# Performance work log

Measured on AMD Instinct MI355X. Metric: run time of the kernel, lower is better.

The kernel has to match this reference:

```python
import jax, jax.numpy as jnp
import numpy as np

N = 10000          # nodes
E = 160000         # edges (before self-loops)
F_IN = 256
H, C = 8, 64       # heads, channels per head
NUM_CLASSES = 40
NEG_SLOPE = 0.2    # PyG GATConv default leaky_relu slope


def setup_inputs() -> dict:
    key = jax.random.key(0)
    ks = jax.random.split(key, 16)
    s = 0.1  # keep logits tame
    x = jax.random.normal(ks[0], (N, F_IN), jnp.float32)
    edge_index = jax.random.randint(ks[1], (2, E), 0, N)
    W0 = jax.random.normal(ks[2], (F_IN, H * C), jnp.float32) / np.sqrt(F_IN)
    a_src0 = jax.random.normal(ks[3], (H, C), jnp.float32) * s
    a_dst0 = jax.random.normal(ks[4], (H, C), jnp.float32) * s
    b0 = jnp.zeros((H * C,), jnp.float32)
    W1 = jax.random.normal(ks[5], (H * C, H * C), jnp.float32) / np.sqrt(H * C)
    a_src1 = jax.random.normal(ks[6], (H, C), jnp.float32) * s
    a_dst1 = jax.random.normal(ks[7], (H, C), jnp.float32) * s
    b1 = jnp.zeros((H * C,), jnp.float32)
    W2 = jax.random.normal(ks[8], (H * C, NUM_CLASSES), jnp.float32) / np.sqrt(H * C)
    a_src2 = jax.random.normal(ks[9], (1, NUM_CLASSES), jnp.float32) * s
    a_dst2 = jax.random.normal(ks[10], (1, NUM_CLASSES), jnp.float32) * s
    b2 = jnp.zeros((NUM_CLASSES,), jnp.float32)
    return dict(x=x, edge_index=edge_index, W0=W0, a_src0=a_src0, a_dst0=a_dst0, b0=b0,
                W1=W1, a_src1=a_src1, a_dst1=a_dst1, b1=b1,
                W2=W2, a_src2=a_src2, a_dst2=a_dst2, b2=b2)


def gat_conv(x, src, dst, W, a_src, a_dst, b, concat):
    """PyG GATConv (eval mode: dropout = identity)."""
    n = x.shape[0]
    h, c = a_src.shape
    hx = (x @ W).reshape(n, h, c)                       # [N,H,C]
    al_s = jnp.sum(hx * a_src, axis=-1)                 # [N,H]
    al_d = jnp.sum(hx * a_dst, axis=-1)                 # [N,H]
    e = jax.nn.leaky_relu(al_s[src] + al_d[dst], NEG_SLOPE)  # [E,H]
    # neighbor softmax over incoming edges of each dst node
    m = jax.ops.segment_max(e, dst, num_segments=n)     # [N,H]
    ex = jnp.exp(e - m[dst])
    denom = jax.ops.segment_sum(ex, dst, num_segments=n)
    alpha = ex / (denom[dst] + 1e-16)                   # [E,H]
    msg = hx[src] * alpha[:, :, None]                   # [E,H,C]
    out = jax.ops.segment_sum(msg, dst, num_segments=n) # [N,H,C]
    out = out.reshape(n, h * c) if concat else out.mean(axis=1)
    return out + b


def reference(x, edge_index, W0, a_src0, a_dst0, b0, W1, a_src1, a_dst1, b1,
              W2, a_src2, a_dst2, b2):
    # add self-loops once (PyG GATConv add_self_loops=True)
    loops = jnp.arange(N, dtype=edge_index.dtype)
    src = jnp.concatenate([edge_index[0], loops])
    dst = jnp.concatenate([edge_index[1], loops])
    x = jax.nn.elu(gat_conv(x, src, dst, W0, a_src0, a_dst0, b0, True))
    x = jax.nn.elu(gat_conv(x, src, dst, W1, a_src1, a_dst1, b1, True))
    return gat_conv(x, src, dst, W2, a_src2, a_dst2, b2, False)
```

## Files before the change

### kernel.cpp

```cpp
#include <hip/hip_runtime.h>
#include <math.h>

#define NN 10000
#define EE 160000
#define ET 170000
#define FIN 256
#define HH 8
#define CC 64
#define HC 512
#define NCLS 40
#define ELLW 96

typedef unsigned short u16;
typedef unsigned int u32;
typedef _Float16 f16;
using f16x8 = __attribute__((ext_vector_type(8))) _Float16;
using f16x4 = __attribute__((ext_vector_type(4))) _Float16;
using f32x4 = __attribute__((ext_vector_type(4))) float;

#define MFMA16(a, b, c) __builtin_amdgcn_mfma_f32_16x16x32_f16((a), (b), (c), 0, 0, 0)

__global__ __launch_bounds__(256) void prep_kernel(const float* __restrict__ x,
                                                   const float* __restrict__ W0,
                                                   const float* __restrict__ W1,
                                                   const float* __restrict__ W2,
                                                   f16* __restrict__ xh,
                                                   f16* __restrict__ w0T,
                                                   f16* __restrict__ w1T,
                                                   f16* __restrict__ w2T,
                                                   int* __restrict__ cnt) {
    int i = blockIdx.x * 256 + threadIdx.x;
    if (i < NN) cnt[i] = 0;
    if (i < NN * FIN / 4) {
        float4 v = ((const float4*)x)[i];
        f16x4 o;
        o[0] = (f16)v.x; o[1] = (f16)v.y; o[2] = (f16)v.z; o[3] = (f16)v.w;
        ((f16x4*)xh)[i] = o;
    } else {
        int j = i - NN * FIN / 4;
        if (j < HC * FIN) {
            int n = j >> 8, k = j & 255;
            w0T[j] = (f16)W0[(size_t)k * HC + n];
        } else if (j < HC * FIN + HC * HC) {
            int q = j - HC * FIN;
            int n = q >> 9, k = q & 511;
            w1T[q] = (f16)W1[(size_t)k * HC + n];
        } else if (j < HC * FIN + HC * HC + NCLS * HC) {
            int q = j - HC * FIN - HC * HC;
            int n = q >> 9, k = q & 511;
            w2T[q] = (f16)W2[(size_t)k * NCLS + n];
        }
    }
}

__global__ __launch_bounds__(256) void scatter_ell(const int* __restrict__ ei,
                                                   int* __restrict__ cnt,
                                                   int* __restrict__ ell) {
    int e = blockIdx.x * 256 + threadIdx.x;
    if (e >= ET) return;
    int s, d;
    if (e < EE) { s = ei[e]; d = ei[EE + e]; }
    else        { s = e - EE; d = s; }
    int pos = atomicAdd(&cnt[d], 1);
    if (pos < ELLW) ell[(size_t)d * ELLW + pos] = s;
}

template <int K>
__global__ __launch_bounds__(512) void gemm_attn(const f16* __restrict__ A,
                                                 const f16* __restrict__ BT,
                                                 const float* __restrict__ a_src,
                                                 const float* __restrict__ a_dst,
                                                 f16* __restrict__ hx2,
                                                 float* __restrict__ al_s,
                                                 float* __restrict__ al_d) {
    constexpr int KK = K / 32;
    constexpr int CH = K / 8;
    __shared__ f16 Bs[64 * K];
    int t = threadIdx.x;
    int hp = blockIdx.x;
    int lane = t & 63, w = t >> 6;
    int fm = lane & 15, g = lane >> 4;
    int bm = blockIdx.y * 128 + w * 16;
    int row = bm + fm;
    bool rok = row < NN;

    f16x8 af[KK];
#pragma unroll
    for (int kk = 0; kk < KK; ++kk) {
        uint4 r = rok ? *(const uint4*)(A + (size_t)row * K + kk * 32 + g * 8)
                      : make_uint4(0u, 0u, 0u, 0u);
        af[kk] = __builtin_bit_cast(f16x8, r);
    }

    for (int sl = 0; sl < 2; ++sl) {
        int h = hp * 2 + sl;
        const f16* bsrc = BT + (size_t)h * 64 * K;
        for (int c = t; c < 64 * CH; c += 512) {
            int brow = c / CH;
            int j = c - brow * CH;
            uint4 v = *(const uint4*)(bsrc + (size_t)brow * K + j * 8);
            *(uint4*)&Bs[(size_t)brow * K + ((j ^ (brow & 7)) * 8)] = v;
        }
        __syncthreads();

        f32x4 acc[4] = {};
#pragma unroll
        for (int kk = 0; kk < KK; ++kk) {
#pragma unroll
            for (int nt = 0; nt < 4; ++nt) {
                f16x8 b = *(const f16x8*)
                    &Bs[(nt * 16 + fm) * K + (((kk * 4 + g) ^ (fm & 7)) * 8)];
                acc[nt] = MFMA16(af[kk], b, acc[nt]);
            }
        }

        float asc[4], adc[4];
#pragma unroll
        for (int nt = 0; nt < 4; ++nt) {
            asc[nt] = a_src[h * 64 + nt * 16 + fm];
            adc[nt] = a_dst[h * 64 + nt * 16 + fm];
        }
#pragma unroll
        for (int r = 0; r < 4; ++r) {
            int orow = bm + g * 4 + r;
            float s = acc[0][r] * asc[0] + acc[1][r] * asc[1] +
                      acc[2][r] * asc[2] + acc[3][r] * asc[3];
            float d = acc[0][r] * adc[0] + acc[1][r] * adc[1] +
                      acc[2][r] * adc[2] + acc[3][r] * adc[3];
#pragma unroll
            for (int off = 1; off < 16; off <<= 1) {
                s += __shfl_xor(s, off);
                d += __shfl_xor(d, off);
            }
            if (orow < NN) {
                if (fm == 0) {
                    al_s[orow * 8 + h] = s;
                    al_d[orow * 8 + h] = d;
                }
#pragma unroll
                for (int nt = 0; nt < 4; ++nt)
                    hx2[(size_t)orow * HC + h * 64 + nt * 16 + fm] =
                        (f16)acc[nt][r];
            }
        }
        __syncthreads();
    }
}

__global__ __launch_bounds__(256) void gemm2_attn(const f16* __restrict__ A,
                                                  const f16* __restrict__ BT,
                                                  const float* __restrict__ a_src2,
                                                  const float* __restrict__ a_dst2,
                                                  float* __restrict__ hx40,
                                                  float* __restrict__ als2,
                                                  float* __restrict__ ald2) {
    __shared__ f16 Bs[48 * HC];
    int t = threadIdx.x;
    int lane = t & 63, w = t >> 6;
    int fm = lane & 15, g = lane >> 4;
    int bm = blockIdx.x * 64 + w * 16;
    int row = bm + fm;
    bool rok = row < NN;

    for (int c = t; c < 48 * 64; c += 256) {
        int brow = c >> 6, j = c & 63;
        uint4 v = make_uint4(0u, 0u, 0u, 0u);
        if (brow < NCLS) v = *(const uint4*)(BT + (size_t)brow * HC + j * 8);
        *(uint4*)&Bs[brow * HC + ((j ^ (brow & 7)) * 8)] = v;
    }

    f16x8 af[16];
#pragma unroll
    for (int kk = 0; kk < 16; ++kk) {
        uint4 r = rok ? *(const uint4*)(A + (size_t)row * HC + kk * 32 + g * 8)
                      : make_uint4(0u, 0u, 0u, 0u);
        af[kk] = __builtin_bit_cast(f16x8, r);
    }
    __syncthreads();

    f32x4 acc[3] = {};
#pragma unroll
    for (int kk = 0; kk < 16; ++kk) {
#pragma unroll
        for (int nt = 0; nt < 3; ++nt) {
            f16x8 b = *(const f16x8*)
                &Bs[(nt * 16 + fm) * HC + (((kk * 4 + g) ^ (fm & 7)) * 8)];
            acc[nt] = MFMA16(af[kk], b, acc[nt]);
        }
    }

    float a2s[3], a2d[3];
#pragma unroll
    for (int nt = 0; nt < 3; ++nt) {
        int col = nt * 16 + fm;
        a2s[nt] = (col < NCLS) ? a_src2[col] : 0.f;
        a2d[nt] = (col < NCLS) ? a_dst2[col] : 0.f;
    }
#pragma unroll
    for (int r = 0; r < 4; ++r) {
        int orow = bm + g * 4 + r;
        float s = acc[0][r] * a2s[0] + acc[1][r] * a2s[1] + acc[2][r] * a2s[2];
        float d = acc[0][r] * a2d[0] + acc[1][r] * a2d[1] + acc[2][r] * a2d[2];
#pragma unroll
        for (int off = 1; off < 16; off <<= 1) {
            s += __shfl_xor(s, off);
            d += __shfl_xor(d, off);
        }
        if (orow < NN) {
            if (fm == 0) { als2[orow] = s; ald2[orow] = d; }
#pragma unroll
            for (int nt = 0; nt < 3; ++nt) {
                int col = nt * 16 + fm;
                if (col < NCLS) hx40[(size_t)orow * NCLS + col] = acc[nt][r];
            }
        }
    }
}

__global__ __launch_bounds__(256) void agg_ell(const f16* __restrict__ hx2,
                                               const float* __restrict__ al_s,
                                               const float* __restrict__ al_d,
                                               const int* __restrict__ cnt,
                                               const int* __restrict__ ell,
                                               const float* __restrict__ bias,
                                               f16* __restrict__ outF) {
    __shared__ float accbuf[2][64][8];
    __shared__ float denbuf[2][64];
    int t = threadIdx.x;
    int lane = t & 63, w = t >> 6;
    int p = w >> 1, sub = w & 1;
    int n = blockIdx.x * 2 + p;
    bool nok = n < NN;
    int ch = lane * 8;
    int h = lane >> 3;
    float acc[8] = {0.f, 0.f, 0.f, 0.f, 0.f, 0.f, 0.f, 0.f};
    float den = 0.f;
    if (nok) {
        float ald = al_d[n * HH + h];
        int dg = cnt[n]; if (dg > ELLW) dg = ELLW;
        const int* ep = ell + (size_t)n * ELLW;
        int nq = dg >> 2;
        for (int q = sub; q < nq; q += 2) {
            int4 ss = *(const int4*)(ep + (q << 2));
            float e0 = al_s[ss.x * HH + h], e1 = al_s[ss.y * HH + h];
            float e2 = al_s[ss.z * HH + h], e3 = al_s[ss.w * HH + h];
            uint4 v0 = *(const uint4*)(hx2 + (size_t)ss.x * HC + ch);
            uint4 v1 = *(const uint4*)(hx2 + (size_t)ss.y * HC + ch);
            uint4 v2 = *(const uint4*)(hx2 + (size_t)ss.z * HC + ch);
            uint4 v3 = *(const uint4*)(hx2 + (size_t)ss.w * HC + ch);
            e0 += ald; e0 = e0 > 0.f ? e0 : 0.2f * e0;
            e1 += ald; e1 = e1 > 0.f ? e1 : 0.2f * e1;
            e2 += ald; e2 = e2 > 0.f ? e2 : 0.2f * e2;
            e3 += ald; e3 = e3 > 0.f ? e3 : 0.2f * e3;
            float w0 = __expf(e0), w1 = __expf(e1);
            float w2 = __expf(e2), w3 = __expf(e3);
            f16x8 f0 = __builtin_bit_cast(f16x8, v0);
            f16x8 f1 = __builtin_bit_cast(f16x8, v1);
            f16x8 f2 = __builtin_bit_cast(f16x8, v2);
            f16x8 f3 = __builtin_bit_cast(f16x8, v3);
#pragma unroll
            for (int j = 0; j < 8; ++j)
                acc[j] += w0 * (float)f0[j] + w1 * (float)f1[j] +
                          w2 * (float)f2[j] + w3 * (float)f3[j];
            den += w0 + w1 + w2 + w3;
        }
        if (sub == (nq & 1)) {
            for (int i = nq << 2; i < dg; ++i) {
                int s = ep[i];
                float e = al_s[s * HH + h] + ald;
                e = e > 0.f ? e : 0.2f * e;
                float wgt = __expf(e);
                uint4 v = *(const uint4*)(hx2 + (size_t)s * HC + ch);
                f16x8 f = __builtin_bit_cast(f16x8, v);
#pragma unroll
                for (int j = 0; j < 8; ++j) acc[j] += wgt * (float)f[j];
                den += wgt;
            }
        }
    }
    if (sub == 1) {
#pragma unroll
        for (int j = 0; j < 8; ++j) accbuf[p][lane][j] = acc[j];
        denbuf[p][lane] = den;
    }
    __syncthreads();
    if (sub == 0 && nok) {
#pragma unroll
        for (int j = 0; j < 8; ++j) acc[j] += accbuf[p][lane][j];
        den += denbuf[p][lane];
        float inv = 1.f / (den + 1e-16f);
        float4 b0v = *(const float4*)(bias + ch);
        float4 b1v = *(const float4*)(bias + ch + 4);
        float bb[8] = {b0v.x, b0v.y, b0v.z, b0v.w, b1v.x, b1v.y, b1v.z, b1v.w};
        f16x8 o;
#pragma unroll
        for (int j = 0; j < 8; ++j) {
            float v = acc[j] * inv + bb[j];
            v = v > 0.f ? v : expm1f(v);
            o[j] = (f16)v;
        }
        *(uint4*)(outF + (size_t)n * HC + ch) = __builtin_bit_cast(uint4, o);
    }
}

__global__ __launch_bounds__(64) void agg2_final(const float* __restrict__ hx40,
                                                 const float* __restrict__ als,
                                                 const float* __restrict__ aldp,
                                                 const int* __restrict__ cnt,
                                                 const int* __restrict__ ell,
                                                 const float* __restrict__ b2,
                                                 float* __restrict__ out) {
    int n = blockIdx.x;
    int c = threadIdx.x;
    float ald = aldp[n];
    int dg = cnt[n]; if (dg > ELLW) dg = ELLW;
    const int* ep = ell + (size_t)n * ELLW;
    float acc = 0.f, den = 0.f;
    int i = 0;
    for (; i + 4 <= dg; i += 4) {
        int4 ss = *(const int4*)(ep + i);
        float e0 = als[ss.x], e1 = als[ss.y], e2 = als[ss.z], e3 = als[ss.w];
        float v0 = 0.f, v1 = 0.f, v2 = 0.f, v3 = 0.f;
        if (c < NCLS) {
            v0 = hx40[(size_t)ss.x * NCLS + c];
            v1 = hx40[(size_t)ss.y * NCLS + c];
            v2 = hx40[(size_t)ss.z * NCLS + c];
            v3 = hx40[(size_t)ss.w * NCLS + c];
        }
        e0 += ald; e0 = e0 > 0.f ? e0 : 0.2f * e0;
        e1 += ald; e1 = e1 > 0.f ? e1 : 0.2f * e1;
        e2 += ald; e2 = e2 > 0.f ? e2 : 0.2f * e2;
        e3 += ald; e3 = e3 > 0.f ? e3 : 0.2f * e3;
        float w0 = __expf(e0), w1 = __expf(e1), w2 = __expf(e2), w3 = __expf(e3);
        acc += w0 * v0 + w1 * v1 + w2 * v2 + w3 * v3;
        den += w0 + w1 + w2 + w3;
    }
    for (; i < dg; ++i) {
        int s = ep[i];
        float e = als[s] + ald;
        e = e > 0.f ? e : 0.2f * e;
        float wgt = __expf(e);
        if (c < NCLS) acc += wgt * hx40[(size_t)s * NCLS + c];
        den += wgt;
    }
    if (c < NCLS) out[(size_t)n * NCLS + c] = acc / (den + 1e-16f) + b2[c];
}

extern "C" void kernel_launch(void* const* d_in, const int* in_sizes, int n_in,
                              void* d_out, int out_size, void* d_ws, size_t ws_size,
                              hipStream_t stream) {
    const float* x   = (const float*)d_in[0];
    const int*   ei  = (const int*)  d_in[1];
    const float* W0  = (const float*)d_in[2];
    const float* as0 = (const float*)d_in[3];
    const float* ad0 = (const float*)d_in[4];
    const float* b0  = (const float*)d_in[5];
    const float* W1  = (const float*)d_in[6];
    const float* as1 = (const float*)d_in[7];
    const float* ad1 = (const float*)d_in[8];
    const float* b1  = (const float*)d_in[9];
    const float* W2  = (const float*)d_in[10];
    const float* as2 = (const float*)d_in[11];
    const float* ad2 = (const float*)d_in[12];
    const float* b2  = (const float*)d_in[13];
    float* out = (float*)d_out;

    char* p = (char*)d_ws;
    int* cnt  = (int*)p; p += 40064;
    int* ell  = (int*)p; p += (size_t)NN * ELLW * 4;
    f16* w0T  = (f16*)p; p += HC * FIN * 2;
    f16* w1T  = (f16*)p; p += HC * HC * 2;
    f16* w2T  = (f16*)p; p += NCLS * HC * 2;
    f16* xh   = (f16*)p; p += (size_t)NN * FIN * 2;
    f16* hxA  = (f16*)p; p += (size_t)NN * HC * 2;
    f16* hxB  = (f16*)p; p += (size_t)NN * HC * 2;
    f16* fA   = (f16*)p; p += (size_t)NN * HC * 2;
    f16* fB   = (f16*)p; p += (size_t)NN * HC * 2;
    float* hx40 = (float*)p; p += (size_t)NN * NCLS * 4;
    float* als0 = (float*)p; p += NN * HH * 4;
    float* ald0 = (float*)p; p += NN * HH * 4;
    float* als1 = (float*)p; p += NN * HH * 4;
    float* ald1 = (float*)p; p += NN * HH * 4;
    float* als2 = (float*)p; p += NN * 4;
    float* ald2 = (float*)p; p += NN * 4;

    const int NBR = (NN + 127) / 128;
    const int NAG = (NN + 1) / 2;
    const int NB2 = (NN + 63) / 64;
    const int PREP = NN * FIN / 4 + HC * FIN + HC * HC + NCLS * HC;

    prep_kernel<<<(PREP + 255) / 256, 256, 0, stream>>>(
        x, W0, W1, W2, xh, w0T, w1T, w2T, cnt);
    scatter_ell<<<(ET + 255) / 256, 256, 0, stream>>>(ei, cnt, ell);

    dim3 gA(4, NBR);
    gemm_attn<FIN><<<gA, 512, 0, stream>>>(xh, w0T, as0, ad0, hxA, als0, ald0);
    agg_ell<<<NAG, 256, 0, stream>>>(hxA, als0, ald0, cnt, ell, b0, fA);
    gemm_attn<HC><<<gA, 512, 0, stream>>>(fA, w1T, as1, ad1, hxB, als1, ald1);
    agg_ell<<<NAG, 256, 0, stream>>>(hxB, als1, ald1, cnt, ell, b1, fB);
    gemm2_attn<<<NB2, 256, 0, stream>>>(fB, w2T, as2, ad2, hx40, als2, ald2);
    agg2_final<<<NN, 64, 0, stream>>>(hx40, als2, ald2, cnt, ell, b2, out);
}
```

Baseline: 206.5 us.

## Split layer aggregation into column slices with intra-wave edge parallelism

Replaces the two-wave-per-node aggregation with a kernel where each wave handles one node and one 128-column slice (two heads), and a 4-slice grid dimension covers all columns. Within a wave, four edge groups of 16 lanes process edges in parallel and are combined with cross-lane shuffles, removing the shared-memory reduction and __syncthreads. This aims to expose more independent gathers per wave and better spread work over CUs. In exchange, each edge's index and attention logit are reloaded per slice, and the grid assumes NN divisible by 4, dropping the bounds check.

```diff
diff --git a/kernel.cpp b/kernel.cpp
--- a/kernel.cpp
+++ b/kernel.cpp
@@ -6,13 +6,10 @@
 #define ET 170000
 #define FIN 256
 #define HH 8
-#define CC 64
 #define HC 512
 #define NCLS 40
 #define ELLW 96
 
-typedef unsigned short u16;
-typedef unsigned int u32;
 typedef _Float16 f16;
 using f16x8 = __attribute__((ext_vector_type(8))) _Float16;
 using f16x4 = __attribute__((ext_vector_type(4))) _Float16;
@@ -217,80 +214,63 @@
     }
 }
 
-__global__ __launch_bounds__(256) void agg_ell(const f16* __restrict__ hx2,
-                                               const float* __restrict__ al_s,
-                                               const float* __restrict__ al_d,
-                                               const int* __restrict__ cnt,
-                                               const int* __restrict__ ell,
-                                               const float* __restrict__ bias,
-                                               f16* __restrict__ outF) {
-    __shared__ float accbuf[2][64][8];
-    __shared__ float denbuf[2][64];
+__global__ __launch_bounds__(256) void agg_slice(const f16* __restrict__ hx2,
+                                                 const float* __restrict__ al_s,
+                                                 const float* __restrict__ al_d,
+                                                 const int* __restrict__ cnt,
+                                                 const int* __restrict__ ell,
+                                                 const float* __restrict__ bias,
+                                                 f16* __restrict__ outF) {
     int t = threadIdx.x;
     int lane = t & 63, w = t >> 6;
-    int p = w >> 1, sub = w & 1;
-    int n = blockIdx.x * 2 + p;
-    bool nok = n < NN;
-    int ch = lane * 8;
-    int h = lane >> 3;
+    int li = lane & 15, eg = lane >> 4;
+    int s = blockIdx.y;
+    int n = blockIdx.x * 4 + w;
+    int h = s * 2 + (li >> 3);
+    int co = s * 128 + li * 8;
+    float ald = al_d[n * HH + h];
+    int dg = cnt[n]; if (dg > ELLW) dg = ELLW;
+    const int* ep = ell + (size_t)n * ELLW;
     float acc[8] = {0.f, 0.f, 0.f, 0.f, 0.f, 0.f, 0.f, 0.f};
     float den = 0.f;
-    if (nok) {
-        float ald = al_d[n * HH + h];
-        int dg = cnt[n]; if (dg > ELLW) dg = ELLW;
-        const int* ep = ell + (size_t)n * ELLW;
-        int nq = dg >> 2;
-        for (int q = sub; q < nq; q += 2) {
-            int4 ss = *(const int4*)(ep + (q << 2));
-            float e0 = al_s[ss.x * HH + h], e1 = al_s[ss.y * HH + h];
-            float e2 = al_s[ss.z * HH + h], e3 = al_s[ss.w * HH + h];
-            uint4 v0 = *(const uint4*)(hx2 + (size_t)ss.x * HC + ch);
-            uint4 v1 = *(const uint4*)(hx2 + (size_t)ss.y * HC + ch);
-            uint4 v2 = *(const uint4*)(hx2 + (size_t)ss.z * HC + ch);
-            uint4 v3 = *(const uint4*)(hx2 + (size_t)ss.w * HC + ch);
-            e0 += ald; e0 = e0 > 0.f ? e0 : 0.2f * e0;
-            e1 += ald; e1 = e1 > 0.f ? e1 : 0.2f * e1;
-            e2 += ald; e2 = e2 > 0.f ? e2 : 0.2f * e2;
-            e3 += ald; e3 = e3 > 0.f ? e3 : 0.2f * e3;
-            float w0 = __expf(e0), w1 = __expf(e1);
-            float w2 = __expf(e2), w3 = __expf(e3);
-            f16x8 f0 = __builtin_bit_cast(f16x8, v0);
-            f16x8 f1 = __builtin_bit_cast(f16x8, v1);
-            f16x8 f2 = __builtin_bit_cast(f16x8, v2);
-            f16x8 f3 = __builtin_bit_cast(f16x8, v3);
-#pragma unroll
-            for (int j = 0; j < 8; ++j)
-                acc[j] += w0 * (float)f0[j] + w1 * (float)f1[j] +
-                          w2 * (float)f2[j] + w3 * (float)f3[j];
-            den += w0 + w1 + w2 + w3;
-        }
-        if (sub == (nq & 1)) {
-            for (int i = nq << 2; i < dg; ++i) {
-                int s = ep[i];
-                float e = al_s[s * HH + h] + ald;
-                e = e > 0.f ? e : 0.2f * e;
-                float wgt = __expf(e);
-                uint4 v = *(const uint4*)(hx2 + (size_t)s * HC + ch);
-                f16x8 f = __builtin_bit_cast(f16x8, v);
-#pragma unroll
-                for (int j = 0; j < 8; ++j) acc[j] += wgt * (float)f[j];
-                den += wgt;
-            }
-        }
-    }
-    if (sub == 1) {
-#pragma unroll
-        for (int j = 0; j < 8; ++j) accbuf[p][lane][j] = acc[j];
-        denbuf[p][lane] = den;
-    }
-    __syncthreads();
-    if (sub == 0 && nok) {
-#pragma unroll
-        for (int j = 0; j < 8; ++j) acc[j] += accbuf[p][lane][j];
-        den += denbuf[p][lane];
+    int i = eg;
+    for (; i + 4 < dg; i += 8) {
+        int s0 = ep[i], s1 = ep[i + 4];
+        float e0 = al_s[s0 * HH + h], e1 = al_s[s1 * HH + h];
+        uint4 v0 = *(const uint4*)(hx2 + (size_t)s0 * HC + co);
+        uint4 v1 = *(const uint4*)(hx2 + (size_t)s1 * HC + co);
+        e0 += ald; e0 = e0 > 0.f ? e0 : 0.2f * e0;
+        e1 += ald; e1 = e1 > 0.f ? e1 : 0.2f * e1;
+        float w0 = __expf(e0), w1 = __expf(e1);
+        f16x8 f0 = __builtin_bit_cast(f16x8, v0);
+        f16x8 f1 = __builtin_bit_cast(f16x8, v1);
+#pragma unroll
+        for (int j = 0; j < 8; ++j)
+            acc[j] += w0 * (float)f0[j] + w1 * (float)f1[j];
+        den += w0 + w1;
+    }
+    if (i < dg) {
+        int s0 = ep[i];
+        float e0 = al_s[s0 * HH + h] + ald;
+        e0 = e0 > 0.f ? e0 : 0.2f * e0;
+        float w0 = __expf(e0);
+        uint4 v0 = *(const uint4*)(hx2 + (size_t)s0 * HC + co);
+        f16x8 f0 = __builtin_bit_cast(f16x8, v0);
+#pragma unroll
+        for (int j = 0; j < 8; ++j) acc[j] += w0 * (float)f0[j];
+        den += w0;
+    }
+#pragma unroll
+    for (int j = 0; j < 8; ++j) {
+        acc[j] += __shfl_xor(acc[j], 16);
+        acc[j] += __shfl_xor(acc[j], 32);
+    }
+    den += __shfl_xor(den, 16);
+    den += __shfl_xor(den, 32);
+    if (eg == 0) {
         float inv = 1.f / (den + 1e-16f);
-        float4 b0v = *(const float4*)(bias + ch);
-        float4 b1v = *(const float4*)(bias + ch + 4);
+        float4 b0v = *(const float4*)(bias + co);
+        float4 b1v = *(const float4*)(bias + co + 4);
         float bb[8] = {b0v.x, b0v.y, b0v.z, b0v.w, b1v.x, b1v.y, b1v.z, b1v.w};
         f16x8 o;
 #pragma unroll
@@ -299,7 +279,7 @@
             v = v > 0.f ? v : expm1f(v);
             o[j] = (f16)v;
         }
-        *(uint4*)(outF + (size_t)n * HC + ch) = __builtin_bit_cast(uint4, o);
+        *(uint4*)(outF + (size_t)n * HC + co) = __builtin_bit_cast(uint4, o);
     }
 }
 
@@ -385,7 +365,6 @@
     float* ald2 = (float*)p; p += NN * 4;
 
     const int NBR = (NN + 127) / 128;
-    const int NAG = (NN + 1) / 2;
     const int NB2 = (NN + 63) / 64;
     const int PREP = NN * FIN / 4 + HC * FIN + HC * HC + NCLS * HC;
 
@@ -394,10 +373,11 @@
     scatter_ell<<<(ET + 255) / 256, 256, 0, stream>>>(ei, cnt, ell);
 
     dim3 gA(4, NBR);
+    dim3 gAg(NN / 4, 4);
     gemm_attn<FIN><<<gA, 512, 0, stream>>>(xh, w0T, as0, ad0, hxA, als0, ald0);
-    agg_ell<<<NAG, 256, 0, stream>>>(hxA, als0, ald0, cnt, ell, b0, fA);
+    agg_slice<<<gAg, 256, 0, stream>>>(hxA, als0, ald0, cnt, ell, b0, fA);
     gemm_attn<HC><<<gA, 512, 0, stream>>>(fA, w1T, as1, ad1, hxB, als1, ald1);
-    agg_ell<<<NAG, 256, 0, stream>>>(hxB, als1, ald1, cnt, ell, b1, fB);
+    agg_slice<<<gAg, 256, 0, stream>>>(hxB, als1, ald1, cnt, ell, b1, fB);
     gemm2_attn<<<NB2, 256, 0, stream>>>(fB, w2T, as2, ad2, hx40, als2, ald2);
     agg2_final<<<NN, 64, 0, stream>>>(hx40, als2, ald2, cnt, ell, b2, out);
 }
```

Result: slower. 218.0 us (+5.6%).
